# Optimization experiments

Hardware: AMD Instinct MI355X
Metric: run time of the kernel (lower is better)

The kernel has to match this reference:

```python
import jax, jax.numpy as jnp
import numpy as np

B, NV, RN, SN = 1, 4, 1024, 128
H = W = 256
C_FEAT = 32   # img_feat_dim
D_VIEW = 32   # view transformer d_model
PE_D = 8      # PE_d_hid
D_RAY = D_VIEW + PE_D  # 40
NHEAD = 8
EPS_LN = 1e-5


def _layernorm(x, g, b):
    m = x.mean(-1, keepdims=True)
    v = ((x - m) ** 2).mean(-1, keepdims=True)
    return (x - m) * jax.lax.rsqrt(v + EPS_LN) * g + b


def _linear_attention(q, k, v):
    # LoFTR kernelized linear attention; q,k,v: (n, L, h, d)
    Q = jax.nn.elu(q) + 1.0
    K = jax.nn.elu(k) + 1.0
    L = v.shape[1]
    KV = jnp.einsum('nshd,nshv->nhdv', K, v / L)
    Z = 1.0 / (jnp.einsum('nlhd,nhd->nlh', Q, K.sum(axis=1)) + 1e-6)
    return jnp.einsum('nlhd,nhdv,nlh->nlhv', Q, KV, Z) * L


def _loftr_self_layer(x, Wq, Wk, Wv, Wm, g1, b1, W1, W2, g2, b2):
    # LoFTREncoderLayer with self-attention (x is both query and source)
    n, L, d = x.shape
    dim = d // NHEAD
    q = (x @ Wq).reshape(n, L, NHEAD, dim)
    k = (x @ Wk).reshape(n, L, NHEAD, dim)
    v = (x @ Wv).reshape(n, L, NHEAD, dim)
    msg = _linear_attention(q, k, v).reshape(n, L, d) @ Wm
    msg = _layernorm(msg, g1, b1)
    msg = jax.nn.relu(jnp.concatenate([x, msg], -1) @ W1) @ W2
    msg = _layernorm(msg, g2, b2)
    return x + msg


def _grid_sample_2d(img, pix):
    # img: (N,C,H,W); pix: (N,RN,SN,2) in pixel coords.
    # bilinear, align_corners=True, zero padding; mask = in-bounds.
    N, C, Hh, Ww = img.shape
    x, y = pix[..., 0], pix[..., 1]
    mask = ((x >= 0) & (x <= Ww - 1) & (y >= 0) & (y <= Hh - 1)).astype(img.dtype)
    x0 = jnp.floor(x)
    y0 = jnp.floor(y)
    flat = img.reshape(N, C, Hh * Ww)

    def gather(ix, iy):
        valid = ((ix >= 0) & (ix < Ww) & (iy >= 0) & (iy < Hh)).astype(img.dtype)
        idx = (jnp.clip(iy, 0, Hh - 1) * Ww + jnp.clip(ix, 0, Ww - 1)).astype(jnp.int32)
        out = jnp.take_along_axis(flat, idx.reshape(N, 1, -1), axis=2)
        return out.reshape(N, C, ix.shape[1], ix.shape[2]) * valid[:, None]

    wx1 = x - x0
    wy1 = y - y0
    out = (gather(x0, y0) * ((1 - wx1) * (1 - wy1))[:, None]
           + gather(x0 + 1, y0) * (wx1 * (1 - wy1))[:, None]
           + gather(x0, y0 + 1) * ((1 - wx1) * wy1)[:, None]
           + gather(x0 + 1, y0 + 1) * (wx1 * wy1)[:, None])
    return out, mask


def _order_posenc(d_hid, n):
    pos = np.arange(n)[:, None].astype(np.float64)
    j = np.arange(d_hid)[None, :]
    tab = pos / np.power(10000.0, 2 * (j // 2) / d_hid)
    tab[:, 0::2] = np.sin(tab[:, 0::2])
    tab[:, 1::2] = np.cos(tab[:, 1::2])
    return jnp.asarray(tab, dtype=jnp.float32)


def _forward(point3D, source_imgs, source_imgs_feat, ref_pose_inv, source_poses_inv,
             source_poses, view_token,
             vt_Wq, vt_Wk, vt_Wv, vt_Wm, vt_g1, vt_b1, vt_W1, vt_W2, vt_g2, vt_b2,
             rt_Wq, rt_Wk, rt_Wv, rt_Wm, rt_g1, rt_b1, rt_W1, rt_W2, rt_g2, rt_b2,
             dm_W1, dm_b1, dm_W2, dm_b2, dm_W3, dm_b3,
             rw_W1, rw_b1, rw_W2, rw_b2, rw_W3, rw_b3):
    b, nv, _, h, w = source_imgs.shape
    _, rn, sn, _ = point3D.shape

    # relative viewing directions (B,NV,RN,SN,3)
    v1 = point3D - ref_pose_inv[:, None, None, :3, -1]
    v2 = point3D[:, None] - source_poses_inv[:, :, None, None, :3, -1]
    v1 = v1 / jnp.linalg.norm(v1, axis=-1, keepdims=True)
    v2 = v2 / jnp.linalg.norm(v2, axis=-1, keepdims=True)
    dir_relative = v1[:, None] - v2

    # project points into all source views: (B,NV,3,RN,SN)
    pts_h = jnp.concatenate([point3D, jnp.ones_like(point3D[..., :1])], -1)
    pip = jnp.einsum('bnij,brsj->bnirs', source_poses, pts_h)[:, :, :3]
    mask_valid_depth = (pip[:, :, 2] > 0).astype(point3D.dtype)
    pix = pip[:, :, :2] / pip[:, :, 2:3]
    grid = jnp.moveaxis(pix, 2, -1).reshape(b * nv, rn, sn, 2)

    feat_s, mask = _grid_sample_2d(source_imgs_feat.reshape(b * nv, -1, h, w), grid)
    rgb_s, _ = _grid_sample_2d(source_imgs.reshape(b * nv, -1, h, w), grid)
    mask = mask.reshape(b, nv, rn, sn) * mask_valid_depth

    # per-point multi-view tokens: (B*RN*SN, NV, C)
    x = feat_s.reshape(b, nv, -1, rn, sn).transpose(0, 3, 4, 1, 2).reshape(b * rn * sn, nv, -1)
    tok = jnp.broadcast_to(view_token, (x.shape[0], 1, view_token.shape[-1]))
    x = jnp.concatenate([tok, x], axis=1)  # prepend view token -> L = NV+1
    x = _loftr_self_layer(x, vt_Wq, vt_Wk, vt_Wv, vt_Wm, vt_g1, vt_b1, vt_W1, vt_W2, vt_g2, vt_b2)

    x1 = jnp.moveaxis(x, 1, 0)          # (NV+1, B*RN*SN, C)
    view_feature = x1[1:]
    x = x1[0].reshape(b * rn, sn, -1)   # token output per sample along ray

    pe = _order_posenc(PE_D, sn)        # (SN, 8)
    x = jnp.concatenate([x, jnp.broadcast_to(pe, (b * rn, sn, PE_D))], -1)
    x = _loftr_self_layer(x, rt_Wq, rt_Wk, rt_Wv, rt_Wm, rt_g1, rt_b1, rt_W1, rt_W2, rt_g2, rt_b2)

    hdm = jax.nn.relu(x @ dm_W1 + dm_b1)
    hdm = jax.nn.relu(hdm @ dm_W2 + dm_b2)
    srdf = hdm @ dm_W3 + dm_b3           # (B*RN, SN, 1)

    # radiance blending weights over views
    vf = view_feature.reshape(nv, b, rn, sn, -1).transpose(1, 2, 3, 0, 4)  # (B,RN,SN,NV,C)
    dr = dir_relative.transpose(0, 2, 3, 1, 4)                             # (B,RN,SN,NV,3)
    xw = jnp.concatenate([vf, dr], -1)
    xw = jax.nn.relu(xw @ rw_W1 + rw_b1)
    xw = jax.nn.relu(xw @ rw_W2 + rw_b2)
    xw = xw @ rw_W3 + rw_b3                                                # (B,RN,SN,NV,1)
    m = mask.transpose(0, 2, 3, 1)[..., None]
    xw = jnp.where(m == 0, -1e9, xw)
    weight = jax.nn.softmax(xw, axis=-2)
    w_bn = weight[..., 0].transpose(0, 3, 1, 2)[:, :, None]                # (B,NV,1,RN,SN)
    radiance = (rgb_s.reshape(b, nv, 3, rn, sn) * w_bn).sum(axis=1)        # (B,3,RN,SN)
    radiance = radiance.transpose(0, 2, 3, 1).reshape(b * rn * sn, 3)
    return radiance, srdf, pip


def setup_inputs() -> dict:
    key = jax.random.key(0)
    ks = jax.random.split(key, 4)
    u = jax.random.uniform(ks[0], (B, RN, SN, 3), dtype=jnp.float32)
    point3D = jnp.concatenate([u[..., :2] - 0.5, u[..., 2:] + 1.0], -1)  # x,y in [-.5,.5], z in [1,2]
    source_imgs = jax.random.normal(ks[1], (B, NV, 3, H, W), dtype=jnp.float32) * 0.5
    source_imgs_feat = jax.random.normal(ks[2], (B, NV, C_FEAT, H, W), dtype=jnp.float32) * 0.5

    f = 200.0
    P = np.array([[f, 0, W / 2, 0], [0, f, H / 2, 0], [0, 0, 1, 0], [0, 0, 0, 1]], np.float32)
    source_poses = jnp.asarray(np.broadcast_to(P, (B, NV, 4, 4)).copy())
    ref_pose_inv = jnp.asarray(np.broadcast_to(np.eye(4, dtype=np.float32), (B, 4, 4)).copy())
    spi = np.broadcast_to(np.eye(4, dtype=np.float32), (B, NV, 4, 4)).copy()
    spi[:, :, 0, 3] = np.linspace(-0.2, 0.2, NV, dtype=np.float32)  # camera centers
    source_poses_inv = jnp.asarray(spi)

    pk = jax.random.split(ks[3], 20)

    def lin(k, i, o):
        return jax.random.normal(k, (i, o), dtype=jnp.float32) * 0.05

    d, dr = D_VIEW, D_RAY
    params = dict(
        view_token=jax.random.normal(pk[0], (1, d), dtype=jnp.float32),
        vt_Wq=lin(pk[1], d, d), vt_Wk=lin(pk[2], d, d), vt_Wv=lin(pk[3], d, d), vt_Wm=lin(pk[4], d, d),
        vt_g1=jnp.ones(d), vt_b1=jnp.zeros(d),
        vt_W1=lin(pk[5], 2 * d, 2 * d), vt_W2=lin(pk[6], 2 * d, d),
        vt_g2=jnp.ones(d), vt_b2=jnp.zeros(d),
        rt_Wq=lin(pk[7], dr, dr), rt_Wk=lin(pk[8], dr, dr), rt_Wv=lin(pk[9], dr, dr), rt_Wm=lin(pk[10], dr, dr),
        rt_g1=jnp.ones(dr), rt_b1=jnp.zeros(dr),
        rt_W1=lin(pk[11], 2 * dr, 2 * dr), rt_W2=lin(pk[12], 2 * dr, dr),
        rt_g2=jnp.ones(dr), rt_b2=jnp.zeros(dr),
        dm_W1=lin(pk[13], dr, 32), dm_b1=jnp.zeros(32),
        dm_W2=lin(pk[14], 32, 16), dm_b2=jnp.zeros(16),
        dm_W3=lin(pk[15], 16, 1), dm_b3=jnp.zeros(1),
        rw_W1=lin(pk[16], d + 3, 16), rw_b1=jnp.zeros(16),
        rw_W2=lin(pk[17], 16, 8), rw_b2=jnp.zeros(8),
        rw_W3=lin(pk[18], 8, 1), rw_b3=jnp.zeros(1),
    )
    out = dict(point3D=point3D, source_imgs=source_imgs, source_imgs_feat=source_imgs_feat,
               ref_pose_inv=ref_pose_inv, source_poses_inv=source_poses_inv,
               source_poses=source_poses)
    out.update(params)
    return out


def reference(point3D, source_imgs, source_imgs_feat, ref_pose_inv, source_poses_inv,
              source_poses, view_token,
              vt_Wq, vt_Wk, vt_Wv, vt_Wm, vt_g1, vt_b1, vt_W1, vt_W2, vt_g2, vt_b2,
              rt_Wq, rt_Wk, rt_Wv, rt_Wm, rt_g1, rt_b1, rt_W1, rt_W2, rt_g2, rt_b2,
              dm_W1, dm_b1, dm_W2, dm_b2, dm_W3, dm_b3,
              rw_W1, rw_b1, rw_W2, rw_b2, rw_W3, rw_b3):
    return _forward(point3D, source_imgs, source_imgs_feat, ref_pose_inv, source_poses_inv,
                    source_poses, view_token,
                    vt_Wq, vt_Wk, vt_Wv, vt_Wm, vt_g1, vt_b1, vt_W1, vt_W2, vt_g2, vt_b2,
                    rt_Wq, rt_Wk, rt_Wv, rt_Wm, rt_g1, rt_b1, rt_W1, rt_W2, rt_g2, rt_b2,
                    dm_W1, dm_b1, dm_W2, dm_b2, dm_W3, dm_b3,
                    rw_W1, rw_b1, rw_W2, rw_b2, rw_W3, rw_b3)
```

## Files before the change

kernel.cpp:

```cpp
#include <hip/hip_runtime.h>
#include <math.h>

#define NPTS   131072
#define NVIEW  4
#define IMH    256
#define IMW    256

#define WS_FEATT   0u
#define WS_IMGT    8388608u
#define WS_X1      9437184u
#define WS_XR      26214400u
#define WS_MSG     31457280u
#define WS_RGB     36700160u
#define WS_DIR     38273024u
#define WS_MASK    39845888u

__device__ __forceinline__ float elup1(float t) { return t > 0.f ? t + 1.f : expf(t); }

__global__ __launch_bounds__(256) void k0_transpose(
    const float* __restrict__ feat, const float* __restrict__ img,
    float* __restrict__ featT, float* __restrict__ imgT)
{
    int tid = blockIdx.x * 256 + threadIdx.x;
    int v = tid >> 16, pix = tid & 65535;
    float buf[32];
#pragma unroll
    for (int c = 0; c < 32; ++c)
        buf[c] = feat[((size_t)(v * 32 + c) << 16) + pix];
    float4* dst = (float4*)(featT + ((size_t)tid << 5));
#pragma unroll
    for (int q = 0; q < 8; ++q)
        dst[q] = make_float4(buf[4*q], buf[4*q+1], buf[4*q+2], buf[4*q+3]);
    float4 rgb;
    rgb.x = img[((size_t)(v * 3 + 0) << 16) + pix];
    rgb.y = img[((size_t)(v * 3 + 1) << 16) + pix];
    rgb.z = img[((size_t)(v * 3 + 2) << 16) + pix];
    rgb.w = 0.f;
    *(float4*)(imgT + ((size_t)tid << 2)) = rgb;
}

__global__ __launch_bounds__(256) void k1_geom_sample(
    const float* __restrict__ p3d, const float* __restrict__ rpi,
    const float* __restrict__ spi, const float* __restrict__ sp,
    const float* __restrict__ featT, const float* __restrict__ imgT,
    float* __restrict__ x1, float* __restrict__ rgbw,
    float* __restrict__ dirw, float* __restrict__ maskw,
    float* __restrict__ outpip)
{
    int tid = blockIdx.x * 256 + threadIdx.x;
    int p = tid >> 2, v = tid & 3;
    float X = p3d[p * 3 + 0], Y = p3d[p * 3 + 1], Z = p3d[p * 3 + 2];

    float a0 = X - rpi[3], a1 = Y - rpi[7], a2 = Z - rpi[11];
    float na = sqrtf(a0 * a0 + a1 * a1 + a2 * a2);
    a0 /= na; a1 /= na; a2 /= na;
    const float* sv = spi + v * 16;
    float b0 = X - sv[3], b1 = Y - sv[7], b2 = Z - sv[11];
    float nb = sqrtf(b0 * b0 + b1 * b1 + b2 * b2);
    b0 /= nb; b1 /= nb; b2 /= nb;
    dirw[(size_t)p * 12 + v * 3 + 0] = a0 - b0;
    dirw[(size_t)p * 12 + v * 3 + 1] = a1 - b1;
    dirw[(size_t)p * 12 + v * 3 + 2] = a2 - b2;

    const float* P = sp + v * 16;
    float pip0 = P[0] * X + P[1] * Y + P[2]  * Z + P[3];
    float pip1 = P[4] * X + P[5] * Y + P[6]  * Z + P[7];
    float pip2 = P[8] * X + P[9] * Y + P[10] * Z + P[11];
    outpip[(size_t)(v * 3 + 0) * NPTS + p] = pip0;
    outpip[(size_t)(v * 3 + 1) * NPTS + p] = pip1;
    outpip[(size_t)(v * 3 + 2) * NPTS + p] = pip2;

    float gx = pip0 / pip2, gy = pip1 / pip2;
    float inb = (gx >= 0.f && gx <= 255.f && gy >= 0.f && gy <= 255.f) ? 1.f : 0.f;
    float mvd = pip2 > 0.f ? 1.f : 0.f;
    maskw[(size_t)p * 4 + v] = inb * mvd;

    float x0f = floorf(gx), y0f = floorf(gy);
    float wx = gx - x0f, wy = gy - y0f;
    int ix0 = (int)x0f, iy0 = (int)y0f;
    float tw[4] = { (1.f-wx)*(1.f-wy), wx*(1.f-wy), (1.f-wx)*wy, wx*wy };
    int tdx[4] = { 0, 1, 0, 1 };
    int tdy[4] = { 0, 0, 1, 1 };

    float facc[32];
#pragma unroll
    for (int c = 0; c < 32; ++c) facc[c] = 0.f;
    float r0 = 0.f, r1 = 0.f, r2 = 0.f;

#pragma unroll
    for (int tno = 0; tno < 4; ++tno) {
        int ix = ix0 + tdx[tno], iy = iy0 + tdy[tno];
        float valid = (ix >= 0 && ix < IMW && iy >= 0 && iy < IMH) ? 1.f : 0.f;
        int cx = min(max(ix, 0), IMW - 1), cy = min(max(iy, 0), IMH - 1);
        float wgt = tw[tno] * valid;
        size_t base = ((size_t)v << 16) + ((size_t)cy << 8) + (size_t)cx;
        const float4* fp = (const float4*)(featT + base * 32);
#pragma unroll
        for (int q = 0; q < 8; ++q) {
            float4 f4 = fp[q];
            facc[4*q+0] += f4.x * wgt; facc[4*q+1] += f4.y * wgt;
            facc[4*q+2] += f4.z * wgt; facc[4*q+3] += f4.w * wgt;
        }
        float4 rp = *(const float4*)(imgT + base * 4);
        r0 += rp.x * wgt; r1 += rp.y * wgt; r2 += rp.z * wgt;
    }

    float4* xd = (float4*)(x1 + ((size_t)p * 4 + v) * 32);
#pragma unroll
    for (int q = 0; q < 8; ++q)
        xd[q] = make_float4(facc[4*q], facc[4*q+1], facc[4*q+2], facc[4*q+3]);
    rgbw[(size_t)p * 12 + v * 3 + 0] = r0;
    rgbw[(size_t)p * 12 + v * 3 + 1] = r1;
    rgbw[(size_t)p * 12 + v * 3 + 2] = r2;
}

#define K2_BLK 128
#define K2_PTS 24

__global__ __launch_bounds__(K2_BLK) void k2_loftr1(
    float* __restrict__ x1g, const float* __restrict__ vtok,
    const float* __restrict__ Wq, const float* __restrict__ Wk,
    const float* __restrict__ Wv, const float* __restrict__ Wm,
    const float* __restrict__ g1v, const float* __restrict__ b1v,
    const float* __restrict__ W1, const float* __restrict__ W2,
    const float* __restrict__ g2v, const float* __restrict__ b2v,
    float* __restrict__ xr)
{
    __shared__ float xs[8 * K2_BLK * 4];
    __shared__ float kvs[8192];

    int t = threadIdx.x;
    int pl = t / 5, l = t - pl * 5;
    bool act = (t < K2_PTS * 5);
    if (!act) { pl = 0; l = 0; }
    int p = blockIdx.x * K2_PTS + pl;
    bool valid = act && (p < NPTS);
    int pload = p < NPTS ? p : NPTS - 1;

    {
        float4 xrow[8];
        if (l == 0) {
            const float4* sv = (const float4*)vtok;
#pragma unroll
            for (int g = 0; g < 8; ++g) xrow[g] = sv[g];
        } else {
            const float4* sv = (const float4*)(x1g + ((size_t)pload * 4 + (l - 1)) * 32);
#pragma unroll
            for (int g = 0; g < 8; ++g) xrow[g] = sv[g];
        }
#pragma unroll
        for (int g = 0; g < 8; ++g)
            *(float4*)&xs[(g * K2_BLK + t) * 4] = xrow[g];
    }

    {
        float acc[32];
#pragma unroll
        for (int j = 0; j < 32; ++j) acc[j] = 0.f;
#pragma unroll 2
        for (int g = 0; g < 8; ++g) {
            float4 xv = *(const float4*)&xs[(g * K2_BLK + t) * 4];
            const float* w0 = Wk + g * 128;
#pragma unroll
            for (int j = 0; j < 32; ++j) acc[j] = fmaf(xv.x, w0[j],      acc[j]);
#pragma unroll
            for (int j = 0; j < 32; ++j) acc[j] = fmaf(xv.y, w0[32 + j], acc[j]);
#pragma unroll
            for (int j = 0; j < 32; ++j) acc[j] = fmaf(xv.z, w0[64 + j], acc[j]);
#pragma unroll
            for (int j = 0; j < 32; ++j) acc[j] = fmaf(xv.w, w0[96 + j], acc[j]);
        }
        if (act) {
            float* krow = &kvs[(pl * 5 + l) * 68];
#pragma unroll
            for (int j = 0; j < 32; j += 4) {
                float4 o4 = make_float4(elup1(acc[j]), elup1(acc[j+1]), elup1(acc[j+2]), elup1(acc[j+3]));
                *(float4*)&krow[j] = o4;
            }
        }
#pragma unroll
        for (int j = 0; j < 32; ++j) acc[j] = 0.f;
#pragma unroll 2
        for (int g = 0; g < 8; ++g) {
            float4 xv = *(const float4*)&xs[(g * K2_BLK + t) * 4];
            const float* w0 = Wv + g * 128;
#pragma unroll
            for (int j = 0; j < 32; ++j) acc[j] = fmaf(xv.x, w0[j],      acc[j]);
#pragma unroll
            for (int j = 0; j < 32; ++j) acc[j] = fmaf(xv.y, w0[32 + j], acc[j]);
#pragma unroll
            for (int j = 0; j < 32; ++j) acc[j] = fmaf(xv.z, w0[64 + j], acc[j]);
#pragma unroll
            for (int j = 0; j < 32; ++j) acc[j] = fmaf(xv.w, w0[96 + j], acc[j]);
        }
        if (act) {
            float* vrow = &kvs[(pl * 5 + l) * 68 + 32];
#pragma unroll
            for (int j = 0; j < 32; j += 4)
                *(float4*)&vrow[j] = make_float4(acc[j], acc[j+1], acc[j+2], acc[j+3]);
        }
    }

    float qv[32];
    {
        float acc[32];
#pragma unroll
        for (int j = 0; j < 32; ++j) acc[j] = 0.f;
#pragma unroll 2
        for (int g = 0; g < 8; ++g) {
            float4 xv = *(const float4*)&xs[(g * K2_BLK + t) * 4];
            const float* w0 = Wq + g * 128;
#pragma unroll
            for (int j = 0; j < 32; ++j) acc[j] = fmaf(xv.x, w0[j],      acc[j]);
#pragma unroll
            for (int j = 0; j < 32; ++j) acc[j] = fmaf(xv.y, w0[32 + j], acc[j]);
#pragma unroll
            for (int j = 0; j < 32; ++j) acc[j] = fmaf(xv.z, w0[64 + j], acc[j]);
#pragma unroll
            for (int j = 0; j < 32; ++j) acc[j] = fmaf(xv.w, w0[96 + j], acc[j]);
        }
#pragma unroll
        for (int j = 0; j < 32; ++j) qv[j] = elup1(acc[j]);
    }
    __syncthreads();

    float ov[32];
    {
#pragma unroll
        for (int h = 0; h < 8; ++h) {
            float kvm[16] = {0,0,0,0,0,0,0,0,0,0,0,0,0,0,0,0};
            float ksum[4] = {0,0,0,0};
#pragma unroll
            for (int l2 = 0; l2 < 5; ++l2) {
                const float* row = &kvs[(pl * 5 + l2) * 68 + h * 4];
                float4 K4 = *(const float4*)row;
                float4 V4 = *(const float4*)(row + 32);
                kvm[0]  = fmaf(K4.x, V4.x, kvm[0]);  kvm[1]  = fmaf(K4.x, V4.y, kvm[1]);
                kvm[2]  = fmaf(K4.x, V4.z, kvm[2]);  kvm[3]  = fmaf(K4.x, V4.w, kvm[3]);
                kvm[4]  = fmaf(K4.y, V4.x, kvm[4]);  kvm[5]  = fmaf(K4.y, V4.y, kvm[5]);
                kvm[6]  = fmaf(K4.y, V4.z, kvm[6]);  kvm[7]  = fmaf(K4.y, V4.w, kvm[7]);
                kvm[8]  = fmaf(K4.z, V4.x, kvm[8]);  kvm[9]  = fmaf(K4.z, V4.y, kvm[9]);
                kvm[10] = fmaf(K4.z, V4.z, kvm[10]); kvm[11] = fmaf(K4.z, V4.w, kvm[11]);
                kvm[12] = fmaf(K4.w, V4.x, kvm[12]); kvm[13] = fmaf(K4.w, V4.y, kvm[13]);
                kvm[14] = fmaf(K4.w, V4.z, kvm[14]); kvm[15] = fmaf(K4.w, V4.w, kvm[15]);
                ksum[0] += K4.x; ksum[1] += K4.y; ksum[2] += K4.z; ksum[3] += K4.w;
            }
            float q0 = qv[h*4], q1 = qv[h*4+1], q2 = qv[h*4+2], q3 = qv[h*4+3];
            float den = 1e-6f + q0*ksum[0] + q1*ksum[1] + q2*ksum[2] + q3*ksum[3];
            float inv = 1.f / den;
#pragma unroll
            for (int d = 0; d < 4; ++d) {
                float num = q0*kvm[d] + q1*kvm[4+d] + q2*kvm[8+d] + q3*kvm[12+d];
                ov[h*4+d] = num * inv;
            }
        }
    }
    __syncthreads();

#pragma unroll
    for (int g = 0; g < 8; ++g)
        *(float4*)&kvs[(g * K2_BLK + t) * 4] = make_float4(ov[4*g], ov[4*g+1], ov[4*g+2], ov[4*g+3]);

    float msg[32];
    {
        float acc[32];
#pragma unroll
        for (int j = 0; j < 32; ++j) acc[j] = 0.f;
#pragma unroll 2
        for (int g = 0; g < 8; ++g) {
            float4 xv = *(const float4*)&kvs[(g * K2_BLK + t) * 4];
            const float* w0 = Wm + g * 128;
#pragma unroll
            for (int j = 0; j < 32; ++j) acc[j] = fmaf(xv.x, w0[j],      acc[j]);
#pragma unroll
            for (int j = 0; j < 32; ++j) acc[j] = fmaf(xv.y, w0[32 + j], acc[j]);
#pragma unroll
            for (int j = 0; j < 32; ++j) acc[j] = fmaf(xv.z, w0[64 + j], acc[j]);
#pragma unroll
            for (int j = 0; j < 32; ++j) acc[j] = fmaf(xv.w, w0[96 + j], acc[j]);
        }
        float s1 = 0.f, s2 = 0.f;
#pragma unroll
        for (int j = 0; j < 32; ++j) { s1 += acc[j]; s2 += acc[j] * acc[j]; }
        float m = s1 * (1.f / 32.f);
        float var = s2 * (1.f / 32.f) - m * m;
        float rs = rsqrtf(var + 1e-5f);
#pragma unroll
        for (int j = 0; j < 32; ++j) msg[j] = (acc[j] - m) * rs * g1v[j] + b1v[j];
    }
#pragma unroll
    for (int g = 0; g < 8; ++g)
        *(float4*)&kvs[(g * K2_BLK + t) * 4] = make_float4(msg[4*g], msg[4*g+1], msg[4*g+2], msg[4*g+3]);

    {
        float acc[64];
#pragma unroll
        for (int j = 0; j < 64; ++j) acc[j] = 0.f;
#pragma unroll 2
        for (int g = 0; g < 8; ++g) {
            float4 xv = *(const float4*)&xs[(g * K2_BLK + t) * 4];
            const float* w0 = W1 + g * 256;
#pragma unroll
            for (int j = 0; j < 64; ++j) acc[j] = fmaf(xv.x, w0[j],       acc[j]);
#pragma unroll
            for (int j = 0; j < 64; ++j) acc[j] = fmaf(xv.y, w0[64 + j],  acc[j]);
#pragma unroll
            for (int j = 0; j < 64; ++j) acc[j] = fmaf(xv.z, w0[128 + j], acc[j]);
#pragma unroll
            for (int j = 0; j < 64; ++j) acc[j] = fmaf(xv.w, w0[192 + j], acc[j]);
        }
#pragma unroll 2
        for (int g = 0; g < 8; ++g) {
            float4 xv = *(const float4*)&kvs[(g * K2_BLK + t) * 4];
            const float* w0 = W1 + 2048 + g * 256;
#pragma unroll
            for (int j = 0; j < 64; ++j) acc[j] = fmaf(xv.x, w0[j],       acc[j]);
#pragma unroll
            for (int j = 0; j < 64; ++j) acc[j] = fmaf(xv.y, w0[64 + j],  acc[j]);
#pragma unroll
            for (int j = 0; j < 64; ++j) acc[j] = fmaf(xv.z, w0[128 + j], acc[j]);
#pragma unroll
            for (int j = 0; j < 64; ++j) acc[j] = fmaf(xv.w, w0[192 + j], acc[j]);
        }
#pragma unroll
        for (int g = 0; g < 16; ++g) {
            float4 h4 = make_float4(fmaxf(acc[4*g], 0.f),   fmaxf(acc[4*g+1], 0.f),
                                    fmaxf(acc[4*g+2], 0.f), fmaxf(acc[4*g+3], 0.f));
            *(float4*)&kvs[(g * K2_BLK + t) * 4] = h4;
        }
    }

    {
        float acc[32];
#pragma unroll
        for (int j = 0; j < 32; ++j) acc[j] = 0.f;
#pragma unroll 2
        for (int g = 0; g < 16; ++g) {
            float4 xv = *(const float4*)&kvs[(g * K2_BLK + t) * 4];
            const float* w0 = W2 + g * 128;
#pragma unroll
            for (int j = 0; j < 32; ++j) acc[j] = fmaf(xv.x, w0[j],      acc[j]);
#pragma unroll
            for (int j = 0; j < 32; ++j) acc[j] = fmaf(xv.y, w0[32 + j], acc[j]);
#pragma unroll
            for (int j = 0; j < 32; ++j) acc[j] = fmaf(xv.z, w0[64 + j], acc[j]);
#pragma unroll
            for (int j = 0; j < 32; ++j) acc[j] = fmaf(xv.w, w0[96 + j], acc[j]);
        }
        float s1 = 0.f, s2 = 0.f;
#pragma unroll
        for (int j = 0; j < 32; ++j) { s1 += acc[j]; s2 += acc[j] * acc[j]; }
        float m = s1 * (1.f / 32.f);
        float var = s2 * (1.f / 32.f) - m * m;
        float rs = rsqrtf(var + 1e-5f);

        if (valid) {
            float y[32];
#pragma unroll
            for (int g = 0; g < 8; ++g) {
                float4 x4 = *(const float4*)&xs[(g * K2_BLK + t) * 4];
                y[4*g]   = x4.x; y[4*g+1] = x4.y; y[4*g+2] = x4.z; y[4*g+3] = x4.w;
            }
#pragma unroll
            for (int j = 0; j < 32; ++j)
                y[j] += (acc[j] - m) * rs * g2v[j] + b2v[j];

            if (l == 0) {
                float4* dst = (float4*)(xr + (size_t)p * 40);
#pragma unroll
                for (int g = 0; g < 8; ++g)
                    dst[g] = make_float4(y[4*g], y[4*g+1], y[4*g+2], y[4*g+3]);
                int sidx = p & 127;
#pragma unroll
                for (int c = 0; c < 8; ++c) {
                    float den = (c < 2) ? 1.f : (c < 4) ? 10.f : (c < 6) ? 100.f : 1000.f;
                    float arg = (float)sidx / den;
                    xr[(size_t)p * 40 + 32 + c] = (c & 1) ? cosf(arg) : sinf(arg);
                }
            } else {
                float4* dst = (float4*)(x1g + ((size_t)p * 4 + (l - 1)) * 32);
#pragma unroll
                for (int g = 0; g < 8; ++g)
                    dst[g] = make_float4(y[4*g], y[4*g+1], y[4*g+2], y[4*g+3]);
            }
        }
    }
}

__global__ __launch_bounds__(320) void k3a_attn(
    const float* __restrict__ xr,
    const float* __restrict__ Wq, const float* __restrict__ Wk,
    const float* __restrict__ Wv, const float* __restrict__ Wm,
    const float* __restrict__ g1, const float* __restrict__ b1,
    float* __restrict__ msg)
{
    __shared__ float kb[5120];
    __shared__ float vb[5120];
    __shared__ float wb[1600];
    __shared__ float kvb[200];
    __shared__ float ksb[40];
    int t = threadIdx.x, r = blockIdx.x;
    const float* xbase = xr + (size_t)r * 5120;
    int lg = t / 40, c = t % 40;

    for (int i = t; i < 1600; i += 320) wb[i] = Wk[i];
    __syncthreads();
    {
        float acc[16];
#pragma unroll
        for (int i = 0; i < 16; ++i) acc[i] = 0.f;
        for (int kk = 0; kk < 40; ++kk) {
            float w = wb[kk * 40 + c];
#pragma unroll
            for (int i = 0; i < 16; ++i) acc[i] += xbase[(lg * 16 + i) * 40 + kk] * w;
        }
#pragma unroll
        for (int i = 0; i < 16; ++i) kb[(lg * 16 + i) * 40 + c] = elup1(acc[i]);
    }
    __syncthreads();
    for (int i = t; i < 1600; i += 320) wb[i] = Wv[i];
    __syncthreads();
    {
        float acc[16];
#pragma unroll
        for (int i = 0; i < 16; ++i) acc[i] = 0.f;
        for (int kk = 0; kk < 40; ++kk) {
            float w = wb[kk * 40 + c];
#pragma unroll
            for (int i = 0; i < 16; ++i) acc[i] += xbase[(lg * 16 + i) * 40 + kk] * w;
        }
#pragma unroll
        for (int i = 0; i < 16; ++i) vb[(lg * 16 + i) * 40 + c] = acc[i];
    }
    __syncthreads();
    if (t < 200) {
        int h = t / 25, e = (t / 5) % 5, d = t % 5;
        float kv = 0.f, ks = 0.f;
        for (int s2 = 0; s2 < 128; ++s2) {
            float kvv = kb[s2 * 40 + h * 5 + e];
            float vv  = vb[s2 * 40 + h * 5 + d];
            kv += kvv * vv; ks += kvv;
        }
        kvb[t] = kv;
        if (d == 0) ksb[h * 5 + e] = ks;
    }
    __syncthreads();
    for (int i = t; i < 1600; i += 320) wb[i] = Wq[i];
    __syncthreads();
    {
        float acc[16];
#pragma unroll
        for (int i = 0; i < 16; ++i) acc[i] = 0.f;
        for (int kk = 0; kk < 40; ++kk) {
            float w = wb[kk * 40 + c];
#pragma unroll
            for (int i = 0; i < 16; ++i) acc[i] += xbase[(lg * 16 + i) * 40 + kk] * w;
        }
#pragma unroll
        for (int i = 0; i < 16; ++i) kb[(lg * 16 + i) * 40 + c] = elup1(acc[i]);
    }
    __syncthreads();
    {
        int h = c / 5, d = c % 5;
#pragma unroll 4
        for (int i = 0; i < 16; ++i) {
            int l = lg * 16 + i;
            float den = 1e-6f, o = 0.f;
#pragma unroll
            for (int e = 0; e < 5; ++e) {
                float q = kb[l * 40 + h * 5 + e];
                den += q * ksb[h * 5 + e];
                o   += q * kvb[h * 25 + e * 5 + d];
            }
            vb[l * 40 + c] = o / den;
        }
    }
    __syncthreads();
    for (int i = t; i < 1600; i += 320) wb[i] = Wm[i];
    __syncthreads();
    {
        float acc[16];
#pragma unroll
        for (int i = 0; i < 16; ++i) acc[i] = 0.f;
        for (int kk = 0; kk < 40; ++kk) {
            float w = wb[kk * 40 + c];
#pragma unroll
            for (int i = 0; i < 16; ++i) acc[i] += vb[(lg * 16 + i) * 40 + kk] * w;
        }
#pragma unroll
        for (int i = 0; i < 16; ++i) kb[(lg * 16 + i) * 40 + c] = acc[i];
    }
    __syncthreads();
    if (t < 128) {
        float s1 = 0.f, s2v = 0.f;
        for (int j = 0; j < 40; ++j) { float x = kb[t * 40 + j]; s1 += x; s2v += x * x; }
        float m = s1 * (1.f / 40.f), va = s2v * (1.f / 40.f) - m * m;
        float rs = rsqrtf(va + 1e-5f);
        for (int j = 0; j < 40; ++j)
            msg[((size_t)r * 128 + t) * 40 + j] = (kb[t * 40 + j] - m) * rs * g1[j] + b1[j];
    }
}

__global__ __launch_bounds__(320) void k3b_ffn(
    float* __restrict__ xr, const float* __restrict__ msg,
    const float* __restrict__ W1, const float* __restrict__ W2,
    const float* __restrict__ g2, const float* __restrict__ b2)
{
    __shared__ float hb[10240];
    __shared__ float wb[3200];
    int t = threadIdx.x, r = blockIdx.x;
    int lg = t / 40, c = t % 40;
    const float* xbase = xr + (size_t)r * 5120;
    const float* mbase = msg + (size_t)r * 5120;

    float hA[16], hB[16];
#pragma unroll
    for (int i = 0; i < 16; ++i) { hA[i] = 0.f; hB[i] = 0.f; }

    for (int i = t; i < 3200; i += 320) wb[i] = W1[i];
    __syncthreads();
    for (int kk = 0; kk < 40; ++kk) {
        float wa = wb[kk * 80 + c], wbb = wb[kk * 80 + c + 40];
#pragma unroll
        for (int i = 0; i < 16; ++i) {
            float xv = xbase[(lg * 16 + i) * 40 + kk];
            hA[i] += xv * wa; hB[i] += xv * wbb;
        }
    }
    __syncthreads();
    for (int i = t; i < 3200; i += 320) wb[i] = W1[3200 + i];
    __syncthreads();
    for (int kk = 0; kk < 40; ++kk) {
        float wa = wb[kk * 80 + c], wbb = wb[kk * 80 + c + 40];
#pragma unroll
        for (int i = 0; i < 16; ++i) {
            float mv = mbase[(lg * 16 + i) * 40 + kk];
            hA[i] += mv * wa; hB[i] += mv * wbb;
        }
    }
#pragma unroll
    for (int i = 0; i < 16; ++i) {
        hb[(lg * 16 + i) * 80 + c]      = fmaxf(hA[i], 0.f);
        hb[(lg * 16 + i) * 80 + c + 40] = fmaxf(hB[i], 0.f);
    }
    __syncthreads();
    for (int i = t; i < 3200; i += 320) wb[i] = W2[i];
    __syncthreads();
    float oa[16];
#pragma unroll
    for (int i = 0; i < 16; ++i) oa[i] = 0.f;
    for (int kk = 0; kk < 80; ++kk) {
        float w = wb[kk * 40 + c];
#pragma unroll
        for (int i = 0; i < 16; ++i) oa[i] += hb[(lg * 16 + i) * 80 + kk] * w;
    }
    __syncthreads();
#pragma unroll
    for (int i = 0; i < 16; ++i) hb[(lg * 16 + i) * 40 + c] = oa[i];
    __syncthreads();
    if (t < 128) {
        float s1 = 0.f, s2v = 0.f;
        for (int j = 0; j < 40; ++j) { float x = hb[t * 40 + j]; s1 += x; s2v += x * x; }
        float m = s1 * (1.f / 40.f), va = s2v * (1.f / 40.f) - m * m;
        float rs = rsqrtf(va + 1e-5f);
        for (int j = 0; j < 40; ++j) {
            float y = xbase[t * 40 + j] + (hb[t * 40 + j] - m) * rs * g2[j] + b2[j];
            xr[(size_t)r * 5120 + t * 40 + j] = y;
        }
    }
}

__global__ __launch_bounds__(256) void k4_dm(
    const float* __restrict__ xr,
    const float* __restrict__ W1, const float* __restrict__ b1,
    const float* __restrict__ W2, const float* __restrict__ b2,
    const float* __restrict__ W3, const float* __restrict__ b3,
    float* __restrict__ out1)
{
    __shared__ float s[1857];
    int t = threadIdx.x;
    for (int i = t; i < 1280; i += 256) s[i] = W1[i];
    if (t < 32) s[1280 + t] = b1[t];
    for (int i = t; i < 512; i += 256) s[1312 + i] = W2[i];
    if (t < 16) { s[1824 + t] = b2[t]; s[1840 + t] = W3[t]; }
    if (t == 0) s[1856] = b3[0];
    __syncthreads();

    int p = blockIdx.x * 256 + t;
    float x[40];
    const float4* xp = (const float4*)(xr + (size_t)p * 40);
#pragma unroll
    for (int i = 0; i < 10; ++i) {
        float4 v4 = xp[i];
        x[4*i] = v4.x; x[4*i+1] = v4.y; x[4*i+2] = v4.z; x[4*i+3] = v4.w;
    }
    float h1[32];
#pragma unroll
    for (int j = 0; j < 32; ++j) h1[j] = s[1280 + j];
    for (int k = 0; k < 40; ++k) {
        float xv = x[k];
#pragma unroll
        for (int j = 0; j < 32; ++j) h1[j] += xv * s[k * 32 + j];
    }
#pragma unroll
    for (int j = 0; j < 32; ++j) h1[j] = fmaxf(h1[j], 0.f);
    float h2[16];
#pragma unroll
    for (int j = 0; j < 16; ++j) h2[j] = s[1824 + j];
    for (int k = 0; k < 32; ++k) {
        float hv = h1[k];
#pragma unroll
        for (int j = 0; j < 16; ++j) h2[j] += hv * s[1312 + k * 16 + j];
    }
    float o = s[1856];
#pragma unroll
    for (int j = 0; j < 16; ++j) o += fmaxf(h2[j], 0.f) * s[1840 + j];
    out1[p] = o;
}

__global__ __launch_bounds__(256) void k5_rw(
    const float* __restrict__ vf, const float* __restrict__ dirw,
    const float* __restrict__ maskw, const float* __restrict__ rgbw,
    const float* __restrict__ W1, const float* __restrict__ b1,
    const float* __restrict__ W2, const float* __restrict__ b2,
    const float* __restrict__ W3, const float* __restrict__ b3,
    float* __restrict__ out0)
{
    __shared__ float s[721];
    int t = threadIdx.x;
    for (int i = t; i < 560; i += 256) s[i] = W1[i];
    if (t < 16) s[560 + t] = b1[t];
    if (t < 128) s[576 + t] = W2[t];
    if (t < 8) { s[704 + t] = b2[t]; s[712 + t] = W3[t]; }
    if (t == 0) s[720] = b3[0];
    __syncthreads();

    int p = blockIdx.x * 256 + t;
    float xw[4];
#pragma unroll
    for (int v = 0; v < 4; ++v) {
        float in[35];
        const float4* vp = (const float4*)(vf + ((size_t)p * 4 + v) * 32);
#pragma unroll
        for (int q = 0; q < 8; ++q) {
            float4 f4 = vp[q];
            in[4*q] = f4.x; in[4*q+1] = f4.y; in[4*q+2] = f4.z; in[4*q+3] = f4.w;
        }
        in[32] = dirw[(size_t)p * 12 + v * 3 + 0];
        in[33] = dirw[(size_t)p * 12 + v * 3 + 1];
        in[34] = dirw[(size_t)p * 12 + v * 3 + 2];
        float h1[16];
#pragma unroll
        for (int j = 0; j < 16; ++j) h1[j] = s[560 + j];
        for (int k = 0; k < 35; ++k) {
            float xv = in[k];
#pragma unroll
            for (int j = 0; j < 16; ++j) h1[j] += xv * s[k * 16 + j];
        }
        float h2[8];
#pragma unroll
        for (int j = 0; j < 8; ++j) h2[j] = s[704 + j];
        for (int k = 0; k < 16; ++k) {
            float hv = fmaxf(h1[k], 0.f);
#pragma unroll
            for (int j = 0; j < 8; ++j) h2[j] += hv * s[576 + k * 8 + j];
        }
        float o = s[720];
#pragma unroll
        for (int j = 0; j < 8; ++j) o += fmaxf(h2[j], 0.f) * s[712 + j];
        xw[v] = (maskw[(size_t)p * 4 + v] == 0.f) ? -1e9f : o;
    }
    float m = fmaxf(fmaxf(xw[0], xw[1]), fmaxf(xw[2], xw[3]));
    float e0 = expf(xw[0] - m), e1 = expf(xw[1] - m), e2 = expf(xw[2] - m), e3 = expf(xw[3] - m);
    float inv = 1.f / (e0 + e1 + e2 + e3);
    float w4[4] = { e0 * inv, e1 * inv, e2 * inv, e3 * inv };
    float r0 = 0.f, r1 = 0.f, r2 = 0.f;
#pragma unroll
    for (int v = 0; v < 4; ++v) {
        r0 += rgbw[(size_t)p * 12 + v * 3 + 0] * w4[v];
        r1 += rgbw[(size_t)p * 12 + v * 3 + 1] * w4[v];
        r2 += rgbw[(size_t)p * 12 + v * 3 + 2] * w4[v];
    }
    out0[(size_t)p * 3 + 0] = r0;
    out0[(size_t)p * 3 + 1] = r1;
    out0[(size_t)p * 3 + 2] = r2;
}

extern "C" void kernel_launch(void* const* d_in, const int* in_sizes, int n_in,
                              void* d_out, int out_size, void* d_ws, size_t ws_size,
                              hipStream_t stream) {
    (void)in_sizes; (void)n_in; (void)out_size; (void)ws_size;
    const float* p3d   = (const float*)d_in[0];
    const float* imgs  = (const float*)d_in[1];
    const float* feat  = (const float*)d_in[2];
    const float* rpi   = (const float*)d_in[3];
    const float* spi   = (const float*)d_in[4];
    const float* sp    = (const float*)d_in[5];
    const float* vtok  = (const float*)d_in[6];
    const float* vtWq  = (const float*)d_in[7];
    const float* vtWk  = (const float*)d_in[8];
    const float* vtWv  = (const float*)d_in[9];
    const float* vtWm  = (const float*)d_in[10];
    const float* vtg1  = (const float*)d_in[11];
    const float* vtb1  = (const float*)d_in[12];
    const float* vtW1  = (const float*)d_in[13];
    const float* vtW2  = (const float*)d_in[14];
    const float* vtg2  = (const float*)d_in[15];
    const float* vtb2  = (const float*)d_in[16];
    const float* rtWq  = (const float*)d_in[17];
    const float* rtWk  = (const float*)d_in[18];
    const float* rtWv  = (const float*)d_in[19];
    const float* rtWm  = (const float*)d_in[20];
    const float* rtg1  = (const float*)d_in[21];
    const float* rtb1  = (const float*)d_in[22];
    const float* rtW1  = (const float*)d_in[23];
    const float* rtW2  = (const float*)d_in[24];
    const float* rtg2  = (const float*)d_in[25];
    const float* rtb2  = (const float*)d_in[26];
    const float* dmW1  = (const float*)d_in[27];
    const float* dmb1  = (const float*)d_in[28];
    const float* dmW2  = (const float*)d_in[29];
    const float* dmb2  = (const float*)d_in[30];
    const float* dmW3  = (const float*)d_in[31];
    const float* dmb3  = (const float*)d_in[32];
    const float* rwW1  = (const float*)d_in[33];
    const float* rwb1  = (const float*)d_in[34];
    const float* rwW2  = (const float*)d_in[35];
    const float* rwb2  = (const float*)d_in[36];
    const float* rwW3  = (const float*)d_in[37];
    const float* rwb3  = (const float*)d_in[38];

    float* out  = (float*)d_out;
    float* out0 = out;
    float* out1 = out + 393216;
    float* out2 = out + 524288;

    float* ws    = (float*)d_ws;
    float* featT = ws + WS_FEATT;
    float* imgT  = ws + WS_IMGT;
    float* x1    = ws + WS_X1;
    float* xr    = ws + WS_XR;
    float* msg   = ws + WS_MSG;
    float* rgbw  = ws + WS_RGB;
    float* dirw  = ws + WS_DIR;
    float* maskw = ws + WS_MASK;

    k0_transpose<<<dim3(1024), dim3(256), 0, stream>>>(feat, imgs, featT, imgT);
    k1_geom_sample<<<dim3(2048), dim3(256), 0, stream>>>(p3d, rpi, spi, sp, featT, imgT,
                                                         x1, rgbw, dirw, maskw, out2);
    int k2_blocks = (NPTS + K2_PTS - 1) / K2_PTS;
    k2_loftr1<<<dim3(k2_blocks), dim3(K2_BLK), 0, stream>>>(x1, vtok, vtWq, vtWk, vtWv, vtWm,
                                                    vtg1, vtb1, vtW1, vtW2, vtg2, vtb2, xr);
    k3a_attn<<<dim3(1024), dim3(320), 0, stream>>>(xr, rtWq, rtWk, rtWv, rtWm, rtg1, rtb1, msg);
    k3b_ffn<<<dim3(1024), dim3(320), 0, stream>>>(xr, msg, rtW1, rtW2, rtg2, rtb2);
    k4_dm<<<dim3(512), dim3(256), 0, stream>>>(xr, dmW1, dmb1, dmW2, dmb2, dmW3, dmb3, out1);
    k5_rw<<<dim3(512), dim3(256), 0, stream>>>(x1, dirw, maskw, rgbw,
                                               rwW1, rwb1, rwW2, rwb2, rwW3, rwb3, out0);
}
```

Measured before the change: 1.252 ms.

## Stage LoFTR weights in shared memory and split the FFN into column halves

In k2_loftr1, each weight matrix (Wq, Wk, Wv, Wm, W2 and 32x32 blocks of W1) is now copied cooperatively into a 4 KB shared buffer before its matvec, instead of every thread reading it from global memory. The 64-wide FFN hidden layer is computed in two 32-column halves, and each half's W2 contribution is accumulated right away. This halves the accumulator register footprint and avoids keeping a 64-float array live. The price is many extra __syncthreads barriers and extra shared-memory traffic and capacity per block.

```diff
diff --git a/kernel.cpp b/kernel.cpp
--- a/kernel.cpp
+++ b/kernel.cpp
@@ -117,6 +117,46 @@
 #define K2_BLK 128
 #define K2_PTS 24
 
+__device__ __forceinline__ void k2_pass32(const float* __restrict__ wb,
+                                          const float* __restrict__ slot,
+                                          float* __restrict__ acc)
+{
+#pragma unroll 2
+    for (int g = 0; g < 8; ++g) {
+        float4 xv = *(const float4*)(slot + g * (K2_BLK * 4));
+        const float* w0 = wb + g * 128;
+#pragma unroll
+        for (int j = 0; j < 32; ++j) acc[j] = fmaf(xv.x, w0[j],      acc[j]);
+#pragma unroll
+        for (int j = 0; j < 32; ++j) acc[j] = fmaf(xv.y, w0[32 + j], acc[j]);
+#pragma unroll
+        for (int j = 0; j < 32; ++j) acc[j] = fmaf(xv.z, w0[64 + j], acc[j]);
+#pragma unroll
+        for (int j = 0; j < 32; ++j) acc[j] = fmaf(xv.w, w0[96 + j], acc[j]);
+    }
+}
+
+__device__ __forceinline__ void k2_ldw1024(float* __restrict__ wbuf,
+                                           const float* __restrict__ W, int t)
+{
+    float4 a = ((const float4*)W)[t * 2];
+    float4 b = ((const float4*)W)[t * 2 + 1];
+    ((float4*)wbuf)[t * 2]     = a;
+    ((float4*)wbuf)[t * 2 + 1] = b;
+}
+
+__device__ __forceinline__ void k2_ldw1blk(float* __restrict__ wbuf,
+                                           const float* __restrict__ W1,
+                                           int k0, int j0, int t)
+{
+    const float* src = W1 + (size_t)(k0 + (t >> 2)) * 64 + j0 + ((t & 3) << 3);
+    float4 a = ((const float4*)src)[0];
+    float4 b = ((const float4*)src)[1];
+    float* dst = wbuf + t * 8;
+    ((float4*)dst)[0] = a;
+    ((float4*)dst)[1] = b;
+}
+
 __global__ __launch_bounds__(K2_BLK) void k2_loftr1(
     float* __restrict__ x1g, const float* __restrict__ vtok,
     const float* __restrict__ Wq, const float* __restrict__ Wk,
@@ -128,6 +168,7 @@
 {
     __shared__ float xs[8 * K2_BLK * 4];
     __shared__ float kvs[8192];
+    __shared__ float wbuf[1024];
 
     int t = threadIdx.x;
     int pl = t / 5, l = t - pl * 5;
@@ -137,6 +178,10 @@
     bool valid = act && (p < NPTS);
     int pload = p < NPTS ? p : NPTS - 1;
 
+    float* myx   = &xs[t * 4];
+    float* slot0 = &kvs[t * 4];
+    float* slot8 = &kvs[8 * K2_BLK * 4 + t * 4];
+
     {
         float4 xrow[8];
         if (l == 0) {
@@ -150,77 +195,45 @@
         }
 #pragma unroll
         for (int g = 0; g < 8; ++g)
-            *(float4*)&xs[(g * K2_BLK + t) * 4] = xrow[g];
-    }
-
-    {
+            *(float4*)(myx + g * (K2_BLK * 4)) = xrow[g];
+    }
+
+    float qv[32];
+    {
+        __syncthreads(); k2_ldw1024(wbuf, Wq, t); __syncthreads();
         float acc[32];
 #pragma unroll
         for (int j = 0; j < 32; ++j) acc[j] = 0.f;
-#pragma unroll 2
-        for (int g = 0; g < 8; ++g) {
-            float4 xv = *(const float4*)&xs[(g * K2_BLK + t) * 4];
-            const float* w0 = Wk + g * 128;
-#pragma unroll
-            for (int j = 0; j < 32; ++j) acc[j] = fmaf(xv.x, w0[j],      acc[j]);
-#pragma unroll
-            for (int j = 0; j < 32; ++j) acc[j] = fmaf(xv.y, w0[32 + j], acc[j]);
-#pragma unroll
-            for (int j = 0; j < 32; ++j) acc[j] = fmaf(xv.z, w0[64 + j], acc[j]);
-#pragma unroll
-            for (int j = 0; j < 32; ++j) acc[j] = fmaf(xv.w, w0[96 + j], acc[j]);
-        }
+        k2_pass32(wbuf, myx, acc);
+#pragma unroll
+        for (int j = 0; j < 32; ++j) qv[j] = elup1(acc[j]);
+    }
+    {
+        __syncthreads(); k2_ldw1024(wbuf, Wk, t); __syncthreads();
+        float acc[32];
+#pragma unroll
+        for (int j = 0; j < 32; ++j) acc[j] = 0.f;
+        k2_pass32(wbuf, myx, acc);
         if (act) {
             float* krow = &kvs[(pl * 5 + l) * 68];
 #pragma unroll
-            for (int j = 0; j < 32; j += 4) {
-                float4 o4 = make_float4(elup1(acc[j]), elup1(acc[j+1]), elup1(acc[j+2]), elup1(acc[j+3]));
-                *(float4*)&krow[j] = o4;
-            }
-        }
+            for (int j = 0; j < 32; j += 4)
+                *(float4*)&krow[j] = make_float4(elup1(acc[j]), elup1(acc[j+1]),
+                                                 elup1(acc[j+2]), elup1(acc[j+3]));
+        }
+    }
+    {
+        __syncthreads(); k2_ldw1024(wbuf, Wv, t); __syncthreads();
+        float acc[32];
 #pragma unroll
         for (int j = 0; j < 32; ++j) acc[j] = 0.f;
-#pragma unroll 2
-        for (int g = 0; g < 8; ++g) {
-            float4 xv = *(const float4*)&xs[(g * K2_BLK + t) * 4];
-            const float* w0 = Wv + g * 128;
-#pragma unroll
-            for (int j = 0; j < 32; ++j) acc[j] = fmaf(xv.x, w0[j],      acc[j]);
-#pragma unroll
-            for (int j = 0; j < 32; ++j) acc[j] = fmaf(xv.y, w0[32 + j], acc[j]);
-#pragma unroll
-            for (int j = 0; j < 32; ++j) acc[j] = fmaf(xv.z, w0[64 + j], acc[j]);
-#pragma unroll
-            for (int j = 0; j < 32; ++j) acc[j] = fmaf(xv.w, w0[96 + j], acc[j]);
-        }
+        k2_pass32(wbuf, myx, acc);
         if (act) {
             float* vrow = &kvs[(pl * 5 + l) * 68 + 32];
 #pragma unroll
             for (int j = 0; j < 32; j += 4)
                 *(float4*)&vrow[j] = make_float4(acc[j], acc[j+1], acc[j+2], acc[j+3]);
         }
-    }
-
-    float qv[32];
-    {
-        float acc[32];
-#pragma unroll
-        for (int j = 0; j < 32; ++j) acc[j] = 0.f;
-#pragma unroll 2
-        for (int g = 0; g < 8; ++g) {
-            float4 xv = *(const float4*)&xs[(g * K2_BLK + t) * 4];
-            const float* w0 = Wq + g * 128;
-#pragma unroll
-            for (int j = 0; j < 32; ++j) acc[j] = fmaf(xv.x, w0[j],      acc[j]);
-#pragma unroll
-            for (int j = 0; j < 32; ++j) acc[j] = fmaf(xv.y, w0[32 + j], acc[j]);
-#pragma unroll
-            for (int j = 0; j < 32; ++j) acc[j] = fmaf(xv.z, w0[64 + j], acc[j]);
-#pragma unroll
-            for (int j = 0; j < 32; ++j) acc[j] = fmaf(xv.w, w0[96 + j], acc[j]);
-        }
-#pragma unroll
-        for (int j = 0; j < 32; ++j) qv[j] = elup1(acc[j]);
     }
     __syncthreads();
 
@@ -249,36 +262,22 @@
             float den = 1e-6f + q0*ksum[0] + q1*ksum[1] + q2*ksum[2] + q3*ksum[3];
             float inv = 1.f / den;
 #pragma unroll
-            for (int d = 0; d < 4; ++d) {
-                float num = q0*kvm[d] + q1*kvm[4+d] + q2*kvm[8+d] + q3*kvm[12+d];
-                ov[h*4+d] = num * inv;
-            }
+            for (int d = 0; d < 4; ++d)
+                ov[h*4+d] = (q0*kvm[d] + q1*kvm[4+d] + q2*kvm[8+d] + q3*kvm[12+d]) * inv;
         }
     }
     __syncthreads();
 
 #pragma unroll
     for (int g = 0; g < 8; ++g)
-        *(float4*)&kvs[(g * K2_BLK + t) * 4] = make_float4(ov[4*g], ov[4*g+1], ov[4*g+2], ov[4*g+3]);
-
-    float msg[32];
-    {
+        *(float4*)(slot0 + g * (K2_BLK * 4)) = make_float4(ov[4*g], ov[4*g+1], ov[4*g+2], ov[4*g+3]);
+
+    {
+        __syncthreads(); k2_ldw1024(wbuf, Wm, t); __syncthreads();
         float acc[32];
 #pragma unroll
         for (int j = 0; j < 32; ++j) acc[j] = 0.f;
-#pragma unroll 2
-        for (int g = 0; g < 8; ++g) {
-            float4 xv = *(const float4*)&kvs[(g * K2_BLK + t) * 4];
-            const float* w0 = Wm + g * 128;
-#pragma unroll
-            for (int j = 0; j < 32; ++j) acc[j] = fmaf(xv.x, w0[j],      acc[j]);
-#pragma unroll
-            for (int j = 0; j < 32; ++j) acc[j] = fmaf(xv.y, w0[32 + j], acc[j]);
-#pragma unroll
-            for (int j = 0; j < 32; ++j) acc[j] = fmaf(xv.z, w0[64 + j], acc[j]);
-#pragma unroll
-            for (int j = 0; j < 32; ++j) acc[j] = fmaf(xv.w, w0[96 + j], acc[j]);
-        }
+        k2_pass32(wbuf, slot0, acc);
         float s1 = 0.f, s2 = 0.f;
 #pragma unroll
         for (int j = 0; j < 32; ++j) { s1 += acc[j]; s2 += acc[j] * acc[j]; }
@@ -286,70 +285,56 @@
         float var = s2 * (1.f / 32.f) - m * m;
         float rs = rsqrtf(var + 1e-5f);
 #pragma unroll
-        for (int j = 0; j < 32; ++j) msg[j] = (acc[j] - m) * rs * g1v[j] + b1v[j];
-    }
-#pragma unroll
-    for (int g = 0; g < 8; ++g)
-        *(float4*)&kvs[(g * K2_BLK + t) * 4] = make_float4(msg[4*g], msg[4*g+1], msg[4*g+2], msg[4*g+3]);
-
-    {
-        float acc[64];
-#pragma unroll
-        for (int j = 0; j < 64; ++j) acc[j] = 0.f;
-#pragma unroll 2
-        for (int g = 0; g < 8; ++g) {
-            float4 xv = *(const float4*)&xs[(g * K2_BLK + t) * 4];
-            const float* w0 = W1 + g * 256;
-#pragma unroll
-            for (int j = 0; j < 64; ++j) acc[j] = fmaf(xv.x, w0[j],       acc[j]);
-#pragma unroll
-            for (int j = 0; j < 64; ++j) acc[j] = fmaf(xv.y, w0[64 + j],  acc[j]);
-#pragma unroll
-            for (int j = 0; j < 64; ++j) acc[j] = fmaf(xv.z, w0[128 + j], acc[j]);
-#pragma unroll
-            for (int j = 0; j < 64; ++j) acc[j] = fmaf(xv.w, w0[192 + j], acc[j]);
-        }
-#pragma unroll 2
-        for (int g = 0; g < 8; ++g) {
-            float4 xv = *(const float4*)&kvs[(g * K2_BLK + t) * 4];
-            const float* w0 = W1 + 2048 + g * 256;
-#pragma unroll
-            for (int j = 0; j < 64; ++j) acc[j] = fmaf(xv.x, w0[j],       acc[j]);
-#pragma unroll
-            for (int j = 0; j < 64; ++j) acc[j] = fmaf(xv.y, w0[64 + j],  acc[j]);
-#pragma unroll
-            for (int j = 0; j < 64; ++j) acc[j] = fmaf(xv.z, w0[128 + j], acc[j]);
-#pragma unroll
-            for (int j = 0; j < 64; ++j) acc[j] = fmaf(xv.w, w0[192 + j], acc[j]);
-        }
-#pragma unroll
-        for (int g = 0; g < 16; ++g) {
-            float4 h4 = make_float4(fmaxf(acc[4*g], 0.f),   fmaxf(acc[4*g+1], 0.f),
-                                    fmaxf(acc[4*g+2], 0.f), fmaxf(acc[4*g+3], 0.f));
-            *(float4*)&kvs[(g * K2_BLK + t) * 4] = h4;
-        }
-    }
+        for (int j = 0; j < 32; j += 4) {
+            float4 m4 = make_float4((acc[j]   - m) * rs * g1v[j]   + b1v[j],
+                                    (acc[j+1] - m) * rs * g1v[j+1] + b1v[j+1],
+                                    (acc[j+2] - m) * rs * g1v[j+2] + b1v[j+2],
+                                    (acc[j+3] - m) * rs * g1v[j+3] + b1v[j+3]);
+            *(float4*)(slot8 + (j >> 2) * (K2_BLK * 4)) = m4;
+        }
+    }
+
+    float oacc[32];
+#pragma unroll
+    for (int j = 0; j < 32; ++j) oacc[j] = 0.f;
 
     {
         float acc[32];
 #pragma unroll
         for (int j = 0; j < 32; ++j) acc[j] = 0.f;
-#pragma unroll 2
-        for (int g = 0; g < 16; ++g) {
-            float4 xv = *(const float4*)&kvs[(g * K2_BLK + t) * 4];
-            const float* w0 = W2 + g * 128;
-#pragma unroll
-            for (int j = 0; j < 32; ++j) acc[j] = fmaf(xv.x, w0[j],      acc[j]);
-#pragma unroll
-            for (int j = 0; j < 32; ++j) acc[j] = fmaf(xv.y, w0[32 + j], acc[j]);
-#pragma unroll
-            for (int j = 0; j < 32; ++j) acc[j] = fmaf(xv.z, w0[64 + j], acc[j]);
-#pragma unroll
-            for (int j = 0; j < 32; ++j) acc[j] = fmaf(xv.w, w0[96 + j], acc[j]);
-        }
+        __syncthreads(); k2_ldw1blk(wbuf, W1, 0, 0, t);  __syncthreads();
+        k2_pass32(wbuf, myx, acc);
+        __syncthreads(); k2_ldw1blk(wbuf, W1, 32, 0, t); __syncthreads();
+        k2_pass32(wbuf, slot8, acc);
+#pragma unroll
+        for (int j = 0; j < 32; j += 4)
+            *(float4*)(slot0 + (j >> 2) * (K2_BLK * 4)) =
+                make_float4(fmaxf(acc[j], 0.f),   fmaxf(acc[j+1], 0.f),
+                            fmaxf(acc[j+2], 0.f), fmaxf(acc[j+3], 0.f));
+        __syncthreads(); k2_ldw1024(wbuf, W2, t); __syncthreads();
+        k2_pass32(wbuf, slot0, oacc);
+    }
+    {
+        float acc[32];
+#pragma unroll
+        for (int j = 0; j < 32; ++j) acc[j] = 0.f;
+        __syncthreads(); k2_ldw1blk(wbuf, W1, 0, 32, t);  __syncthreads();
+        k2_pass32(wbuf, myx, acc);
+        __syncthreads(); k2_ldw1blk(wbuf, W1, 32, 32, t); __syncthreads();
+        k2_pass32(wbuf, slot8, acc);
+#pragma unroll
+        for (int j = 0; j < 32; j += 4)
+            *(float4*)(slot0 + (j >> 2) * (K2_BLK * 4)) =
+                make_float4(fmaxf(acc[j], 0.f),   fmaxf(acc[j+1], 0.f),
+                            fmaxf(acc[j+2], 0.f), fmaxf(acc[j+3], 0.f));
+        __syncthreads(); k2_ldw1024(wbuf, W2 + 1024, t); __syncthreads();
+        k2_pass32(wbuf, slot0, oacc);
+    }
+
+    {
         float s1 = 0.f, s2 = 0.f;
 #pragma unroll
-        for (int j = 0; j < 32; ++j) { s1 += acc[j]; s2 += acc[j] * acc[j]; }
+        for (int j = 0; j < 32; ++j) { s1 += oacc[j]; s2 += oacc[j] * oacc[j]; }
         float m = s1 * (1.f / 32.f);
         float var = s2 * (1.f / 32.f) - m * m;
         float rs = rsqrtf(var + 1e-5f);
@@ -358,12 +343,12 @@
             float y[32];
 #pragma unroll
             for (int g = 0; g < 8; ++g) {
-                float4 x4 = *(const float4*)&xs[(g * K2_BLK + t) * 4];
+                float4 x4 = *(const float4*)(myx + g * (K2_BLK * 4));
                 y[4*g]   = x4.x; y[4*g+1] = x4.y; y[4*g+2] = x4.z; y[4*g+3] = x4.w;
             }
 #pragma unroll
             for (int j = 0; j < 32; ++j)
-                y[j] += (acc[j] - m) * rs * g2v[j] + b2v[j];
+                y[j] += (oacc[j] - m) * rs * g2v[j] + b2v[j];
 
             if (l == 0) {
                 float4* dst = (float4*)(xr + (size_t)p * 40);
```

Measured after the change: 1.581 ms. +26.3%, slower.
